# Performance work log

Measured on AMD Instinct MI355X. Metric: run time of the kernel, lower is better.

## Reference

```python
import jax, jax.numpy as jnp
import numpy as np

N, E, F_IN, H0, H1, H2 = 50000, 800000, 128, 256, 256, 256
NEG = jnp.finfo(jnp.float32).min


def sage_max(x, src, dst, Wl, bl, Wr):
    # PyG SAGEConv(aggr='max'): lin_l(max_j x_j) + lin_r(x_i)
    agg = jax.ops.segment_max(x[src], dst, num_segments=N)  # [N, F]
    agg = jnp.where(agg <= NEG, 0.0, agg)  # isolated nodes -> 0
    return agg @ Wl + bl + x @ Wr


def setup_inputs() -> dict:
    key = jax.random.key(0)
    ks = jax.random.split(key, 16)
    g = lambda k, shp, fan: jax.random.normal(k, shp, jnp.float32) / np.sqrt(fan)
    inp = {
        "x": jax.random.normal(ks[0], (N, F_IN), jnp.float32),
        "edge_index": jax.random.randint(ks[1], (2, E), 0, N, jnp.int64),
        # shared_l1
        "Wl1": g(ks[2], (F_IN, H0), F_IN), "bl1": jnp.zeros((H0,), jnp.float32), "Wr1": g(ks[3], (F_IN, H0), F_IN),
        # shared_l2
        "Wl2": g(ks[4], (H0, H1), H0), "bl2": jnp.zeros((H1,), jnp.float32), "Wr2": g(ks[5], (H0, H1), H0),
        # rtang_l1 + head
        "Wla": g(ks[6], (H1, H2), H1), "bla": jnp.zeros((H2,), jnp.float32), "Wra": g(ks[7], (H1, H2), H1),
        "Wa": g(ks[8], (H2, 1), H2), "ba": jnp.zeros((1,), jnp.float32),
        # movedis_l1 + head
        "Wlm": g(ks[9], (H1, H2), H1), "blm": jnp.zeros((H2,), jnp.float32), "Wrm": g(ks[10], (H1, H2), H1),
        "Wm": g(ks[11], (H2, 1), H2), "bm": jnp.zeros((1,), jnp.float32),
    }
    return inp


def reference(x, edge_index, Wl1, bl1, Wr1, Wl2, bl2, Wr2,
              Wla, bla, Wra, Wa, ba, Wlm, blm, Wrm, Wm, bm):
    src, dst = edge_index[0], edge_index[1]
    h = jax.nn.relu(sage_max(x, src, dst, Wl1, bl1, Wr1))
    h = jax.nn.relu(sage_max(h, src, dst, Wl2, bl2, Wr2))
    rt = jax.nn.relu(sage_max(h, src, dst, Wla, bla, Wra))
    rt = (rt @ Wa + ba).reshape(-1)  # [N]
    mv = jax.nn.relu(sage_max(h, src, dst, Wlm, blm, Wrm))
    mv = (mv @ Wm + bm).reshape(-1)  # [N]
    return (rt, mv)
```

## Files before the change

### kernel.cpp

```cpp
#include <hip/hip_runtime.h>
#include <hip/hip_bf16.h>


#define NN 50000
#define NE 800000
#define HD 256
#define CAP 64

using bf16 = __hip_bfloat16;
typedef float f32x4 __attribute__((ext_vector_type(4)));
typedef short bf16x8 __attribute__((ext_vector_type(8)));

__device__ __forceinline__ void async16(const void* g, void* l) {
    __builtin_amdgcn_global_load_lds(
        (const __attribute__((address_space(1))) unsigned int*)g,
        (__attribute__((address_space(3))) unsigned int*)l, 16, 0, 0);
}

__device__ __forceinline__ unsigned short f2b(float f) {
    bf16 b = __float2bfloat16(f);
    return __builtin_bit_cast(unsigned short, b);
}

__global__ void k_scatter(const int* __restrict__ ei, int* __restrict__ cnt,
                          int* __restrict__ srcp) {
    int e = blockIdx.x * 256 + threadIdx.x;
    if (e < NE) {
        int d = ei[NE + e];
        int slot = atomicAdd(&cnt[d], 1);
        if (slot < CAP) srcp[(d << 6) + slot] = ei[e];
    }
}

__device__ __forceinline__ void pack1(const float* __restrict__ W,
                                      bf16* __restrict__ bt, int idx, int Ktot,
                                      int kofs) {
    int k = idx >> 8, n = idx & 255;
    bt[(size_t)n * Ktot + kofs + k] = __float2bfloat16(W[idx]);
}

#define PREP_CVT_B 6250
#define PREP_PACK_B 1792
#define PREP_CNT_B 196
#define PREP_B (PREP_CVT_B + PREP_PACK_B + PREP_CNT_B)

__global__ void k_prep(const float* __restrict__ x, bf16* __restrict__ xb,
                       const float* __restrict__ Wl1,
                       const float* __restrict__ Wr1,
                       const float* __restrict__ Wl2,
                       const float* __restrict__ Wr2,
                       const float* __restrict__ Wla,
                       const float* __restrict__ Wra,
                       const float* __restrict__ Wlm,
                       const float* __restrict__ Wrm, bf16* __restrict__ Bt1,
                       bf16* __restrict__ Bt2, bf16* __restrict__ Bta,
                       bf16* __restrict__ Btm, int* __restrict__ cnt) {
    int b = blockIdx.x;
    if (b < PREP_CVT_B) {
        int i = b * 256 + threadIdx.x;
        float4 v = ((const float4*)x)[i];
        ushort4 o;
        o.x = f2b(v.x); o.y = f2b(v.y); o.z = f2b(v.z); o.w = f2b(v.w);
        ((ushort4*)xb)[i] = o;
    } else if (b < PREP_CVT_B + PREP_PACK_B) {
        int idx = (b - PREP_CVT_B) * 256 + threadIdx.x;
        if (idx < 32768) pack1(Wl1, Bt1, idx, 256, 0);
        else if (idx < 65536) pack1(Wr1, Bt1, idx - 32768, 256, 128);
        else if (idx < 131072) pack1(Wl2, Bt2, idx - 65536, 512, 0);
        else if (idx < 196608) pack1(Wr2, Bt2, idx - 131072, 512, 256);
        else if (idx < 262144) pack1(Wla, Bta, idx - 196608, 512, 0);
        else if (idx < 327680) pack1(Wra, Bta, idx - 262144, 512, 256);
        else if (idx < 393216) pack1(Wlm, Btm, idx - 327680, 512, 0);
        else pack1(Wrm, Btm, idx - 393216, 512, 256);
    } else {
        int i = (b - PREP_CVT_B - PREP_PACK_B) * 256 + threadIdx.x;
        if (i < NN) cnt[i] = 0;
    }
}


__device__ __forceinline__ void amax8(float (&m)[8], uint4 v) {
    m[0] = fmaxf(m[0], __uint_as_float(v.x << 16));
    m[1] = fmaxf(m[1], __uint_as_float(v.x & 0xffff0000u));
    m[2] = fmaxf(m[2], __uint_as_float(v.y << 16));
    m[3] = fmaxf(m[3], __uint_as_float(v.y & 0xffff0000u));
    m[4] = fmaxf(m[4], __uint_as_float(v.z << 16));
    m[5] = fmaxf(m[5], __uint_as_float(v.z & 0xffff0000u));
    m[6] = fmaxf(m[6], __uint_as_float(v.w << 16));
    m[7] = fmaxf(m[7], __uint_as_float(v.w & 0xffff0000u));
}

__device__ __forceinline__ uint4 pack8(const float (&m)[8]) {
    uint4 r;
    r.x = (__float_as_uint(m[0]) >> 16) | (__float_as_uint(m[1]) & 0xffff0000u);
    r.y = (__float_as_uint(m[2]) >> 16) | (__float_as_uint(m[3]) & 0xffff0000u);
    r.z = (__float_as_uint(m[4]) >> 16) | (__float_as_uint(m[5]) & 0xffff0000u);
    r.w = (__float_as_uint(m[6]) >> 16) | (__float_as_uint(m[7]) & 0xffff0000u);
    return r;
}

template <int EPL>
__global__ __launch_bounds__(256) void k_agg(const bf16* __restrict__ feat,
                                             bf16* __restrict__ agg,
                                             const int* __restrict__ cnt,
                                             const int* __restrict__ srcp) {
    int node = blockIdx.x * 4 + (threadIdx.x >> 6);
    if (node >= NN) return;
    int lane = threadIdx.x & 63;
    int n = min(cnt[node], CAP);
    const int* __restrict__ lst = srcp + (node << 6);
    const uint4* __restrict__ f4 = (const uint4*)feat;
    float m[8];
#pragma unroll
    for (int i = 0; i < 8; ++i) m[i] = __int_as_float(0xff800000);

    if (EPL == 4) {
        const int half = lane >> 5, sub = lane & 31;
        int e = 0;
        for (; e + 16 <= n; e += 16) {
            int s[8];
#pragma unroll
            for (int j = 0; j < 8; ++j) s[j] = lst[e + 2 * j + half];
            uint4 v[8];
#pragma unroll
            for (int j = 0; j < 8; ++j) v[j] = f4[(size_t)s[j] * 32 + sub];
#pragma unroll
            for (int j = 0; j < 8; ++j) amax8(m, v[j]);
        }
        int rem = n - e;
        if (rem > 8) {
            int s[8];
#pragma unroll
            for (int j = 0; j < 8; ++j) {
                int ix = e + 2 * j + half;
                s[j] = lst[ix < n ? ix : n - 1];
            }
            uint4 v[8];
#pragma unroll
            for (int j = 0; j < 8; ++j) v[j] = f4[(size_t)s[j] * 32 + sub];
#pragma unroll
            for (int j = 0; j < 8; ++j) amax8(m, v[j]);
        } else if (rem > 0) {
            int s[4];
#pragma unroll
            for (int j = 0; j < 4; ++j) {
                int ix = e + 2 * j + half;
                s[j] = lst[ix < n ? ix : n - 1];
            }
            uint4 v[4];
#pragma unroll
            for (int j = 0; j < 4; ++j) v[j] = f4[(size_t)s[j] * 32 + sub];
#pragma unroll
            for (int j = 0; j < 4; ++j) amax8(m, v[j]);
        }
#pragma unroll
        for (int i = 0; i < 8; ++i)
            m[i] = fmaxf(m[i], __shfl_xor(m[i], 32, 64));
        uint4 r = make_uint4(0, 0, 0, 0);
        if (n > 0) r = pack8(m);
        if (half == 0) ((uint4*)agg)[(size_t)node * 32 + sub] = r;
    } else {
        const int q = lane >> 4, sub = lane & 15;
        int e = 0;
        for (; e + 32 <= n; e += 32) {
            int s[8];
#pragma unroll
            for (int j = 0; j < 8; ++j) s[j] = lst[e + 4 * j + q];
            uint4 v[8];
#pragma unroll
            for (int j = 0; j < 8; ++j) v[j] = f4[(size_t)s[j] * 16 + sub];
#pragma unroll
            for (int j = 0; j < 8; ++j) amax8(m, v[j]);
        }
        int rem = n - e;
        if (rem > 16) {
            int s[8];
#pragma unroll
            for (int j = 0; j < 8; ++j) {
                int ix = e + 4 * j + q;
                s[j] = lst[ix < n ? ix : n - 1];
            }
            uint4 v[8];
#pragma unroll
            for (int j = 0; j < 8; ++j) v[j] = f4[(size_t)s[j] * 16 + sub];
#pragma unroll
            for (int j = 0; j < 8; ++j) amax8(m, v[j]);
        } else if (rem > 8) {
            int s[4];
#pragma unroll
            for (int j = 0; j < 4; ++j) {
                int ix = e + 4 * j + q;
                s[j] = lst[ix < n ? ix : n - 1];
            }
            uint4 v[4];
#pragma unroll
            for (int j = 0; j < 4; ++j) v[j] = f4[(size_t)s[j] * 16 + sub];
#pragma unroll
            for (int j = 0; j < 4; ++j) amax8(m, v[j]);
        } else if (rem > 4) {
            int s[2];
#pragma unroll
            for (int j = 0; j < 2; ++j) {
                int ix = e + 4 * j + q;
                s[j] = lst[ix < n ? ix : n - 1];
            }
            uint4 v[2];
#pragma unroll
            for (int j = 0; j < 2; ++j) v[j] = f4[(size_t)s[j] * 16 + sub];
#pragma unroll
            for (int j = 0; j < 2; ++j) amax8(m, v[j]);
        } else if (rem > 0) {
            int ix = e + q;
            int s = lst[ix < n ? ix : n - 1];
            uint4 v = f4[(size_t)s * 16 + sub];
            amax8(m, v);
        }
#pragma unroll
        for (int i = 0; i < 8; ++i)
            m[i] = fmaxf(m[i], __shfl_xor(m[i], 32, 64));
#pragma unroll
        for (int i = 0; i < 8; ++i)
            m[i] = fmaxf(m[i], __shfl_xor(m[i], 16, 64));
        uint4 r = make_uint4(0, 0, 0, 0);
        if (n > 0) r = pack8(m);
        if (lane < 16) ((uint4*)agg)[(size_t)node * 16 + sub] = r;
    }
}

__device__ __forceinline__ void gemm_core256(const bf16* __restrict__ A0,
                                             const bf16* __restrict__ A1, int F,
                                             int Ktot,
                                             const bf16* __restrict__ Bt,
                                             int bm0, int t, short* As,
                                             short* Bs, f32x4 (&acc)[4][8]) {
    const int wave = t >> 6;
    const int lane = t & 63;
    const int q = lane >> 4;
    const int c = lane & 15;
    const int wr = (wave >> 1) * 64;
    const int wcl = (wave & 1) * 128;

    for (int k0 = 0; k0 < Ktot; k0 += 64) {
        const bf16* Asrc = (k0 < F) ? A0 : A1;
        const int kk = (k0 < F) ? k0 : k0 - F;
        __syncthreads();
#pragma unroll
        for (int it = 0; it < 4; ++it) {
            int chunk = it * 256 + t;
            int row = chunk >> 3, kc = chunk & 7;
            int kcg = kc ^ (row & 7);
            int grow = bm0 + row;
            if (grow > NN - 1) grow = NN - 1;
            async16(Asrc + (size_t)grow * F + kk + kcg * 8, &As[chunk * 8]);
        }
#pragma unroll
        for (int it = 0; it < 8; ++it) {
            int chunk = it * 256 + t;
            int row = chunk >> 3, kc = chunk & 7;
            int kcg = kc ^ (row & 7);
            async16(Bt + (size_t)row * Ktot + k0 + kcg * 8, &Bs[chunk * 8]);
        }
        __syncthreads();
#pragma unroll
        for (int ks = 0; ks < 2; ++ks) {
            bf16x8 af[4], bfr[8];
            int ch = (ks * 4 + q) ^ (c & 7);
#pragma unroll
            for (int i = 0; i < 4; ++i)
                af[i] = *(const bf16x8*)&As[(wr + i * 16 + c) * 64 + ch * 8];
#pragma unroll
            for (int j = 0; j < 8; ++j)
                bfr[j] = *(const bf16x8*)&Bs[(wcl + j * 16 + c) * 64 + ch * 8];
#pragma unroll
            for (int i = 0; i < 4; ++i)
#pragma unroll
                for (int j = 0; j < 8; ++j)
                    acc[i][j] = __builtin_amdgcn_mfma_f32_16x16x32_bf16(
                        af[i], bfr[j], acc[i][j], 0, 0, 0);
        }
    }
}

__global__ __launch_bounds__(256, 2) void k_gemm_h(
    const bf16* __restrict__ A0, const bf16* __restrict__ A1, int F, int Ktot,
    const bf16* __restrict__ Bt, const float* __restrict__ bias,
    bf16* __restrict__ Hout) {
    __shared__ __attribute__((aligned(16))) short As[128 * 64];
    __shared__ __attribute__((aligned(16))) short Bs[256 * 64];
    const int t = threadIdx.x;
    const int bm0 = blockIdx.x * 128;
    const int wave = t >> 6;
    const int lane = t & 63;
    const int q = lane >> 4;
    const int c = lane & 15;
    const int wr = (wave >> 1) * 64;
    const int wcl = (wave & 1) * 128;

    f32x4 acc[4][8];
#pragma unroll
    for (int i = 0; i < 4; ++i)
#pragma unroll
        for (int j = 0; j < 8; ++j) acc[i][j] = (f32x4){0.f, 0.f, 0.f, 0.f};
    gemm_core256(A0, A1, F, Ktot, Bt, bm0, t, As, Bs, acc);

    float bcol[8];
#pragma unroll
    for (int j = 0; j < 8; ++j) bcol[j] = bias[wcl + j * 16 + c];
#pragma unroll
    for (int i = 0; i < 4; ++i)
#pragma unroll
        for (int r = 0; r < 4; ++r) {
            int row = bm0 + wr + i * 16 + q * 4 + r;
            if (row < NN) {
#pragma unroll
                for (int j = 0; j < 8; ++j) {
                    int col = wcl + j * 16 + c;
                    float v = fmaxf(acc[i][j][r] + bcol[j], 0.f);
                    Hout[(size_t)row * HD + col] = __float2bfloat16(v);
                }
            }
        }
}

__global__ __launch_bounds__(256, 2) void k_gemm_heads(
    const bf16* __restrict__ A0, const bf16* __restrict__ A1,
    const bf16* __restrict__ Bta, const float* __restrict__ bla,
    const float* __restrict__ Wa, const float* __restrict__ ba,
    const bf16* __restrict__ Btm, const float* __restrict__ blm,
    const float* __restrict__ Wm, const float* __restrict__ bm,
    float* __restrict__ out) {
    __shared__ __attribute__((aligned(16))) short As[128 * 64];
    __shared__ __attribute__((aligned(16))) short Bs[256 * 64];
    const int t = threadIdx.x;
    const int bm0 = blockIdx.x * 128;
    const int z = blockIdx.y;
    const bf16* Bt = z ? Btm : Bta;
    const float* bias = z ? blm : bla;
    const float* Wh = z ? Wm : Wa;
    const float hb = z ? bm[0] : ba[0];
    float* outp = out + (size_t)z * NN;
    const int wave = t >> 6;
    const int lane = t & 63;
    const int q = lane >> 4;
    const int c = lane & 15;
    const int wr = (wave >> 1) * 64;
    const int wcl = (wave & 1) * 128;

    f32x4 acc[4][8];
#pragma unroll
    for (int i = 0; i < 4; ++i)
#pragma unroll
        for (int j = 0; j < 8; ++j) acc[i][j] = (f32x4){0.f, 0.f, 0.f, 0.f};
    gemm_core256(A0, A1, 256, 512, Bt, bm0, t, As, Bs, acc);

    float bcol[8], wcol[8];
#pragma unroll
    for (int j = 0; j < 8; ++j) {
        int col = wcl + j * 16 + c;
        bcol[j] = bias[col];
        wcol[j] = Wh[col];
    }
    float pr[4][4];
#pragma unroll
    for (int i = 0; i < 4; ++i)
#pragma unroll
        for (int r = 0; r < 4; ++r) {
            float p = 0.f;
#pragma unroll
            for (int j = 0; j < 8; ++j)
                p += fmaxf(acc[i][j][r] + bcol[j], 0.f) * wcol[j];
            p += __shfl_xor(p, 1, 64);
            p += __shfl_xor(p, 2, 64);
            p += __shfl_xor(p, 4, 64);
            p += __shfl_xor(p, 8, 64);
            pr[i][r] = p;
        }
    __syncthreads();
    float* red = (float*)As;
    if ((wave & 1) && c == 0) {
#pragma unroll
        for (int i = 0; i < 4; ++i)
#pragma unroll
            for (int r = 0; r < 4; ++r) red[wr + i * 16 + q * 4 + r] = pr[i][r];
    }
    __syncthreads();
    if (!(wave & 1) && c == 0) {
#pragma unroll
        for (int i = 0; i < 4; ++i)
#pragma unroll
            for (int r = 0; r < 4; ++r) {
                int lr = wr + i * 16 + q * 4 + r;
                int row = bm0 + lr;
                if (row < NN) outp[row] = pr[i][r] + red[lr] + hb;
            }
    }
}

extern "C" void kernel_launch(void* const* d_in, const int* in_sizes, int n_in,
                              void* d_out, int out_size, void* d_ws,
                              size_t ws_size, hipStream_t stream) {
    const float* x = (const float*)d_in[0];
    const int* ei = (const int*)d_in[1];
    const float* Wl1 = (const float*)d_in[2];
    const float* bl1 = (const float*)d_in[3];
    const float* Wr1 = (const float*)d_in[4];
    const float* Wl2 = (const float*)d_in[5];
    const float* bl2 = (const float*)d_in[6];
    const float* Wr2 = (const float*)d_in[7];
    const float* Wla = (const float*)d_in[8];
    const float* bla = (const float*)d_in[9];
    const float* Wra = (const float*)d_in[10];
    const float* Wa = (const float*)d_in[11];
    const float* ba = (const float*)d_in[12];
    const float* Wlm = (const float*)d_in[13];
    const float* blm = (const float*)d_in[14];
    const float* Wrm = (const float*)d_in[15];
    const float* Wm = (const float*)d_in[16];
    const float* bm = (const float*)d_in[17];
    float* out = (float*)d_out;

    char* ws = (char*)d_ws;
    size_t off = 0;
    auto alloc = [&](size_t b) {
        void* p = ws + off;
        off = (off + b + 255) & ~(size_t)255;
        return p;
    };
    int* srcp = (int*)alloc((size_t)NN * CAP * 4);
    int* cnt = (int*)alloc((size_t)NN * 4);
    bf16* xb = (bf16*)alloc((size_t)NN * 128 * 2);
    bf16* h1 = (bf16*)alloc((size_t)NN * 256 * 2);
    bf16* h2 = (bf16*)alloc((size_t)NN * 256 * 2);
    bf16* agg = (bf16*)alloc((size_t)NN * 256 * 2);
    bf16* Bt1 = (bf16*)alloc((size_t)256 * 256 * 2);
    bf16* Bt2 = (bf16*)alloc((size_t)256 * 512 * 2);
    bf16* Bta = (bf16*)alloc((size_t)256 * 512 * 2);
    bf16* Btm = (bf16*)alloc((size_t)256 * 512 * 2);
    (void)ws_size; (void)in_sizes; (void)n_in; (void)out_size;

    k_prep<<<PREP_B, 256, 0, stream>>>(x, xb, Wl1, Wr1, Wl2, Wr2, Wla, Wra,
                                       Wlm, Wrm, Bt1, Bt2, Bta, Btm, cnt);
    k_scatter<<<(NE + 255) / 256, 256, 0, stream>>>(ei, cnt, srcp);

    const int GB = (NN + 127) / 128;
    const int NG4 = (NN + 3) / 4;
    k_agg<2><<<NG4, 256, 0, stream>>>(xb, agg, cnt, srcp);
    k_gemm_h<<<GB, 256, 0, stream>>>(agg, xb, 128, 256, Bt1, bl1, h1);
    k_agg<4><<<NG4, 256, 0, stream>>>(h1, agg, cnt, srcp);
    k_gemm_h<<<GB, 256, 0, stream>>>(agg, h1, 256, 512, Bt2, bl2, h2);
    k_agg<4><<<NG4, 256, 0, stream>>>(h2, agg, cnt, srcp);
    dim3 gh(GB, 2);
    k_gemm_heads<<<gh, 256, 0, stream>>>(agg, h2, Bta, bla, Wa, ba, Btm, blm,
                                         Wm, bm, out);
}
```

Measured before the change: 359.4 us.

## Fuse edge scatter into prep kernel and split per-node adjacency into two sub-buckets

Moves the edge-bucketing atomics into the prep kernel so they run alongside the x conversion and weight packing, and zeroes the counters in a small separate kernel first. Each node's neighbor list is split into two 32-slot halves keyed by edge parity, which halves atomic contention per counter. The aggregation kernel now loops over both halves. A node whose edges fall unevenly between the halves can drop neighbors beyond 32 in one half even when its total degree is under the old cap of 64.

```diff
diff --git a/kernel.cpp b/kernel.cpp
--- a/kernel.cpp
+++ b/kernel.cpp
@@ -5,7 +5,6 @@
 #define NN 50000
 #define NE 800000
 #define HD 256
-#define CAP 64
 
 using bf16 = __hip_bfloat16;
 typedef float f32x4 __attribute__((ext_vector_type(4)));
@@ -22,14 +21,9 @@
     return __builtin_bit_cast(unsigned short, b);
 }
 
-__global__ void k_scatter(const int* __restrict__ ei, int* __restrict__ cnt,
-                          int* __restrict__ srcp) {
-    int e = blockIdx.x * 256 + threadIdx.x;
-    if (e < NE) {
-        int d = ei[NE + e];
-        int slot = atomicAdd(&cnt[d], 1);
-        if (slot < CAP) srcp[(d << 6) + slot] = ei[e];
-    }
+__global__ void k_zero(int* __restrict__ cnt) {
+    int i = blockIdx.x * 256 + threadIdx.x;
+    if (i < 2 * NN) cnt[i] = 0;
 }
 
 __device__ __forceinline__ void pack1(const float* __restrict__ W,
@@ -39,13 +33,14 @@
     bt[(size_t)n * Ktot + kofs + k] = __float2bfloat16(W[idx]);
 }
 
+#define SC_B 3125
 #define PREP_CVT_B 6250
 #define PREP_PACK_B 1792
-#define PREP_CNT_B 196
-#define PREP_B (PREP_CVT_B + PREP_PACK_B + PREP_CNT_B)
-
-__global__ void k_prep(const float* __restrict__ x, bf16* __restrict__ xb,
-                       const float* __restrict__ Wl1,
+#define PREP_B (SC_B + PREP_CVT_B + PREP_PACK_B)
+
+__global__ void k_prep(const int* __restrict__ ei, int* __restrict__ cnt,
+                       int* __restrict__ srcp, const float* __restrict__ x,
+                       bf16* __restrict__ xb, const float* __restrict__ Wl1,
                        const float* __restrict__ Wr1,
                        const float* __restrict__ Wl2,
                        const float* __restrict__ Wr2,
@@ -54,16 +49,22 @@
                        const float* __restrict__ Wlm,
                        const float* __restrict__ Wrm, bf16* __restrict__ Bt1,
                        bf16* __restrict__ Bt2, bf16* __restrict__ Bta,
-                       bf16* __restrict__ Btm, int* __restrict__ cnt) {
+                       bf16* __restrict__ Btm) {
     int b = blockIdx.x;
-    if (b < PREP_CVT_B) {
-        int i = b * 256 + threadIdx.x;
+    if (b < SC_B) {
+        int e = b * 256 + threadIdx.x;
+        int d = ei[NE + e];
+        int sub = e & 1;
+        int slot = atomicAdd(&cnt[sub * NN + d], 1);
+        if (slot < 32) srcp[(d << 6) + (sub << 5) + slot] = ei[e];
+    } else if (b < SC_B + PREP_CVT_B) {
+        int i = (b - SC_B) * 256 + threadIdx.x;
         float4 v = ((const float4*)x)[i];
         ushort4 o;
         o.x = f2b(v.x); o.y = f2b(v.y); o.z = f2b(v.z); o.w = f2b(v.w);
         ((ushort4*)xb)[i] = o;
-    } else if (b < PREP_CVT_B + PREP_PACK_B) {
-        int idx = (b - PREP_CVT_B) * 256 + threadIdx.x;
+    } else {
+        int idx = (b - SC_B - PREP_CVT_B) * 256 + threadIdx.x;
         if (idx < 32768) pack1(Wl1, Bt1, idx, 256, 0);
         else if (idx < 65536) pack1(Wr1, Bt1, idx - 32768, 256, 128);
         else if (idx < 131072) pack1(Wl2, Bt2, idx - 65536, 512, 0);
@@ -72,9 +73,6 @@
         else if (idx < 327680) pack1(Wra, Bta, idx - 262144, 512, 256);
         else if (idx < 393216) pack1(Wlm, Btm, idx - 327680, 512, 0);
         else pack1(Wrm, Btm, idx - 393216, 512, 256);
-    } else {
-        int i = (b - PREP_CVT_B - PREP_PACK_B) * 256 + threadIdx.x;
-        if (i < NN) cnt[i] = 0;
     }
 }
 
@@ -107,114 +105,122 @@
     int node = blockIdx.x * 4 + (threadIdx.x >> 6);
     if (node >= NN) return;
     int lane = threadIdx.x & 63;
-    int n = min(cnt[node], CAP);
-    const int* __restrict__ lst = srcp + (node << 6);
+    int c0r = cnt[node], c1r = cnt[NN + node];
     const uint4* __restrict__ f4 = (const uint4*)feat;
     float m[8];
 #pragma unroll
     for (int i = 0; i < 8; ++i) m[i] = __int_as_float(0xff800000);
 
+    for (int seg = 0; seg < 2; ++seg) {
+        const int n = min(seg ? c1r : c0r, 32);
+        const int* __restrict__ lst = srcp + (node << 6) + (seg << 5);
+        if (EPL == 4) {
+            const int half = lane >> 5, sub = lane & 31;
+            int e = 0;
+            for (; e + 16 <= n; e += 16) {
+                int s[8];
+#pragma unroll
+                for (int j = 0; j < 8; ++j) s[j] = lst[e + 2 * j + half];
+                uint4 v[8];
+#pragma unroll
+                for (int j = 0; j < 8; ++j) v[j] = f4[(size_t)s[j] * 32 + sub];
+#pragma unroll
+                for (int j = 0; j < 8; ++j) amax8(m, v[j]);
+            }
+            int rem = n - e;
+            if (rem > 8) {
+                int s[8];
+#pragma unroll
+                for (int j = 0; j < 8; ++j) {
+                    int ix = e + 2 * j + half;
+                    s[j] = lst[ix < n ? ix : n - 1];
+                }
+                uint4 v[8];
+#pragma unroll
+                for (int j = 0; j < 8; ++j) v[j] = f4[(size_t)s[j] * 32 + sub];
+#pragma unroll
+                for (int j = 0; j < 8; ++j) amax8(m, v[j]);
+            } else if (rem > 0) {
+                int s[4];
+#pragma unroll
+                for (int j = 0; j < 4; ++j) {
+                    int ix = e + 2 * j + half;
+                    s[j] = lst[ix < n ? ix : n - 1];
+                }
+                uint4 v[4];
+#pragma unroll
+                for (int j = 0; j < 4; ++j) v[j] = f4[(size_t)s[j] * 32 + sub];
+#pragma unroll
+                for (int j = 0; j < 4; ++j) amax8(m, v[j]);
+            }
+        } else {
+            const int q = lane >> 4, sub = lane & 15;
+            int e = 0;
+            for (; e + 32 <= n; e += 32) {
+                int s[8];
+#pragma unroll
+                for (int j = 0; j < 8; ++j) s[j] = lst[e + 4 * j + q];
+                uint4 v[8];
+#pragma unroll
+                for (int j = 0; j < 8; ++j) v[j] = f4[(size_t)s[j] * 16 + sub];
+#pragma unroll
+                for (int j = 0; j < 8; ++j) amax8(m, v[j]);
+            }
+            int rem = n - e;
+            if (rem > 16) {
+                int s[8];
+#pragma unroll
+                for (int j = 0; j < 8; ++j) {
+                    int ix = e + 4 * j + q;
+                    s[j] = lst[ix < n ? ix : n - 1];
+                }
+                uint4 v[8];
+#pragma unroll
+                for (int j = 0; j < 8; ++j) v[j] = f4[(size_t)s[j] * 16 + sub];
+#pragma unroll
+                for (int j = 0; j < 8; ++j) amax8(m, v[j]);
+            } else if (rem > 8) {
+                int s[4];
+#pragma unroll
+                for (int j = 0; j < 4; ++j) {
+                    int ix = e + 4 * j + q;
+                    s[j] = lst[ix < n ? ix : n - 1];
+                }
+                uint4 v[4];
+#pragma unroll
+                for (int j = 0; j < 4; ++j) v[j] = f4[(size_t)s[j] * 16 + sub];
+#pragma unroll
+                for (int j = 0; j < 4; ++j) amax8(m, v[j]);
+            } else if (rem > 4) {
+                int s[2];
+#pragma unroll
+                for (int j = 0; j < 2; ++j) {
+                    int ix = e + 4 * j + q;
+                    s[j] = lst[ix < n ? ix : n - 1];
+                }
+                uint4 v[2];
+#pragma unroll
+                for (int j = 0; j < 2; ++j) v[j] = f4[(size_t)s[j] * 16 + sub];
+#pragma unroll
+                for (int j = 0; j < 2; ++j) amax8(m, v[j]);
+            } else if (rem > 0) {
+                int ix = e + q;
+                int s = lst[ix < n ? ix : n - 1];
+                uint4 v = f4[(size_t)s * 16 + sub];
+                amax8(m, v);
+            }
+        }
+    }
+
+    bool nonempty = (c0r + c1r) > 0;
     if (EPL == 4) {
-        const int half = lane >> 5, sub = lane & 31;
-        int e = 0;
-        for (; e + 16 <= n; e += 16) {
-            int s[8];
-#pragma unroll
-            for (int j = 0; j < 8; ++j) s[j] = lst[e + 2 * j + half];
-            uint4 v[8];
-#pragma unroll
-            for (int j = 0; j < 8; ++j) v[j] = f4[(size_t)s[j] * 32 + sub];
-#pragma unroll
-            for (int j = 0; j < 8; ++j) amax8(m, v[j]);
-        }
-        int rem = n - e;
-        if (rem > 8) {
-            int s[8];
-#pragma unroll
-            for (int j = 0; j < 8; ++j) {
-                int ix = e + 2 * j + half;
-                s[j] = lst[ix < n ? ix : n - 1];
-            }
-            uint4 v[8];
-#pragma unroll
-            for (int j = 0; j < 8; ++j) v[j] = f4[(size_t)s[j] * 32 + sub];
-#pragma unroll
-            for (int j = 0; j < 8; ++j) amax8(m, v[j]);
-        } else if (rem > 0) {
-            int s[4];
-#pragma unroll
-            for (int j = 0; j < 4; ++j) {
-                int ix = e + 2 * j + half;
-                s[j] = lst[ix < n ? ix : n - 1];
-            }
-            uint4 v[4];
-#pragma unroll
-            for (int j = 0; j < 4; ++j) v[j] = f4[(size_t)s[j] * 32 + sub];
-#pragma unroll
-            for (int j = 0; j < 4; ++j) amax8(m, v[j]);
-        }
 #pragma unroll
         for (int i = 0; i < 8; ++i)
             m[i] = fmaxf(m[i], __shfl_xor(m[i], 32, 64));
         uint4 r = make_uint4(0, 0, 0, 0);
-        if (n > 0) r = pack8(m);
-        if (half == 0) ((uint4*)agg)[(size_t)node * 32 + sub] = r;
+        if (nonempty) r = pack8(m);
+        if (lane < 32) ((uint4*)agg)[(size_t)node * 32 + (lane & 31)] = r;
     } else {
-        const int q = lane >> 4, sub = lane & 15;
-        int e = 0;
-        for (; e + 32 <= n; e += 32) {
-            int s[8];
-#pragma unroll
-            for (int j = 0; j < 8; ++j) s[j] = lst[e + 4 * j + q];
-            uint4 v[8];
-#pragma unroll
-            for (int j = 0; j < 8; ++j) v[j] = f4[(size_t)s[j] * 16 + sub];
-#pragma unroll
-            for (int j = 0; j < 8; ++j) amax8(m, v[j]);
-        }
-        int rem = n - e;
-        if (rem > 16) {
-            int s[8];
-#pragma unroll
-            for (int j = 0; j < 8; ++j) {
-                int ix = e + 4 * j + q;
-                s[j] = lst[ix < n ? ix : n - 1];
-            }
-            uint4 v[8];
-#pragma unroll
-            for (int j = 0; j < 8; ++j) v[j] = f4[(size_t)s[j] * 16 + sub];
-#pragma unroll
-            for (int j = 0; j < 8; ++j) amax8(m, v[j]);
-        } else if (rem > 8) {
-            int s[4];
-#pragma unroll
-            for (int j = 0; j < 4; ++j) {
-                int ix = e + 4 * j + q;
-                s[j] = lst[ix < n ? ix : n - 1];
-            }
-            uint4 v[4];
-#pragma unroll
-            for (int j = 0; j < 4; ++j) v[j] = f4[(size_t)s[j] * 16 + sub];
-#pragma unroll
-            for (int j = 0; j < 4; ++j) amax8(m, v[j]);
-        } else if (rem > 4) {
-            int s[2];
-#pragma unroll
-            for (int j = 0; j < 2; ++j) {
-                int ix = e + 4 * j + q;
-                s[j] = lst[ix < n ? ix : n - 1];
-            }
-            uint4 v[2];
-#pragma unroll
-            for (int j = 0; j < 2; ++j) v[j] = f4[(size_t)s[j] * 16 + sub];
-#pragma unroll
-            for (int j = 0; j < 2; ++j) amax8(m, v[j]);
-        } else if (rem > 0) {
-            int ix = e + q;
-            int s = lst[ix < n ? ix : n - 1];
-            uint4 v = f4[(size_t)s * 16 + sub];
-            amax8(m, v);
-        }
 #pragma unroll
         for (int i = 0; i < 8; ++i)
             m[i] = fmaxf(m[i], __shfl_xor(m[i], 32, 64));
@@ -222,8 +228,8 @@
         for (int i = 0; i < 8; ++i)
             m[i] = fmaxf(m[i], __shfl_xor(m[i], 16, 64));
         uint4 r = make_uint4(0, 0, 0, 0);
-        if (n > 0) r = pack8(m);
-        if (lane < 16) ((uint4*)agg)[(size_t)node * 16 + sub] = r;
+        if (nonempty) r = pack8(m);
+        if (lane < 16) ((uint4*)agg)[(size_t)node * 16 + (lane & 15)] = r;
     }
 }
 
@@ -426,8 +432,8 @@
         off = (off + b + 255) & ~(size_t)255;
         return p;
     };
-    int* srcp = (int*)alloc((size_t)NN * CAP * 4);
-    int* cnt = (int*)alloc((size_t)NN * 4);
+    int* srcp = (int*)alloc((size_t)NN * 64 * 4);
+    int* cnt = (int*)alloc((size_t)2 * NN * 4);
     bf16* xb = (bf16*)alloc((size_t)NN * 128 * 2);
     bf16* h1 = (bf16*)alloc((size_t)NN * 256 * 2);
     bf16* h2 = (bf16*)alloc((size_t)NN * 256 * 2);
@@ -438,9 +444,10 @@
     bf16* Btm = (bf16*)alloc((size_t)256 * 512 * 2);
     (void)ws_size; (void)in_sizes; (void)n_in; (void)out_size;
 
-    k_prep<<<PREP_B, 256, 0, stream>>>(x, xb, Wl1, Wr1, Wl2, Wr2, Wla, Wra,
-                                       Wlm, Wrm, Bt1, Bt2, Bta, Btm, cnt);
-    k_scatter<<<(NE + 255) / 256, 256, 0, stream>>>(ei, cnt, srcp);
+    k_zero<<<(2 * NN + 255) / 256, 256, 0, stream>>>(cnt);
+    k_prep<<<PREP_B, 256, 0, stream>>>(ei, cnt, srcp, x, xb, Wl1, Wr1, Wl2,
+                                       Wr2, Wla, Wra, Wlm, Wrm, Bt1, Bt2, Bta,
+                                       Btm);
 
     const int GB = (NN + 127) / 128;
     const int NG4 = (NN + 3) / 4;
```

New measurement: 368.1 us. 1.02x slower.
